# Kernel optimization log

Measured on AMD Instinct MI355X. Metric: run time of the kernel, lower is better.

The kernel has to match this reference:

```python
import jax, jax.numpy as jnp
import numpy as np

# Keras GRUCell math (reset_after=True default), weights SHARED across all
# num_layers stacked cells (faithful to `[self.rnn_cell for _ in range(L)]`).
NUM_LAYERS = 3
HID = 128


def setup_inputs() -> dict:
    key = jax.random.key(0)
    ks = jax.random.split(key, 4)
    B, T, D, H = 64, 2048, HID, HID
    s = 1.0 / np.sqrt(H)
    return {
        "X": jax.random.uniform(ks[0], (B, T, D), dtype=jnp.float32),
        "kernel": jax.random.normal(ks[1], (D, 3 * H), dtype=jnp.float32) * s,
        "rec_kernel": jax.random.normal(ks[2], (H, 3 * H), dtype=jnp.float32) * s,
        "bias_in": jnp.zeros((3 * H,), dtype=jnp.float32),
        "bias_rec": jnp.zeros((3 * H,), dtype=jnp.float32),
        "W_out": jax.random.normal(ks[3], (H, H), dtype=jnp.float32) * s,
        "b_out": jnp.zeros((H,), dtype=jnp.float32),
    }


def _gru_layer(seq_tbd, kernel, rec_kernel, bias_in, bias_rec):
    # seq_tbd: [T, B, D] -> [T, B, H]
    H = rec_kernel.shape[0]
    B = seq_tbd.shape[1]

    def step(h, x):
        gx = x @ kernel + bias_in            # [B, 3H]
        gh = h @ rec_kernel + bias_rec       # [B, 3H]
        xz, xr, xh = jnp.split(gx, 3, axis=-1)
        hz, hr, hh = jnp.split(gh, 3, axis=-1)
        z = jax.nn.sigmoid(xz + hz)          # update gate
        r = jax.nn.sigmoid(xr + hr)          # reset gate
        cand = jnp.tanh(xh + r * hh)         # candidate state
        h_new = z * h + (1.0 - z) * cand
        return h_new, h_new

    h0 = jnp.zeros((B, H), dtype=seq_tbd.dtype)
    _, out = jax.lax.scan(step, h0, seq_tbd)
    return out


def reference(X, kernel, rec_kernel, bias_in, bias_rec, W_out, b_out):
    seq = jnp.transpose(X, (1, 0, 2))  # [T, B, D]
    for _ in range(NUM_LAYERS):
        seq = _gru_layer(seq, kernel, rec_kernel, bias_in, bias_rec)
    out = jnp.transpose(seq, (1, 0, 2))  # [B, T, H]
    return jax.nn.sigmoid(out @ W_out + b_out)
```

## Files before the change

### kernel.cpp

```cpp
#include <hip/hip_runtime.h>
#include <stdint.h>

#define TSEQ 2048
#define NB   64
#define HD   128
#define G3   384
#define W_RING 128
#define SLOT_U32 (16*128)
#define RING_BYTES ((size_t)12 * W_RING * SLOT_U32 * 4)
#define FLAGS_OFF RING_BYTES

typedef __bf16 bf16_t;
typedef __bf16 bf16x8 __attribute__((ext_vector_type(8)));
typedef float  f32x4  __attribute__((ext_vector_type(4)));
typedef unsigned long long ull;

union B8 { uint4 u; bf16x8 v; unsigned a4[4]; };
union HU { bf16_t h; unsigned short u; };
static_assert(sizeof(B8) == 16, "B8 must be 16B");

__device__ __forceinline__ float fast_sigmoid(float x) {
    float e = __builtin_amdgcn_exp2f(-1.44269504f * x);
    return __builtin_amdgcn_rcpf(1.0f + e);
}
__device__ __forceinline__ float fast_tanh(float x) {
    x = fminf(9.0f, fmaxf(-9.0f, x));
    float e = __builtin_amdgcn_exp2f(2.88539008f * x);
    return 1.0f - 2.0f * __builtin_amdgcn_rcpf(1.0f + e);
}

#define MFMA16(A_, B_, C_) (C_) = __builtin_amdgcn_mfma_f32_16x16x32_bf16((A_), (B_), (C_), 0, 0, 0)

__device__ __forceinline__ void fast_barrier() {
    asm volatile("s_waitcnt lgkmcnt(0)\n\ts_barrier" ::: "memory");
}
__device__ __forceinline__ void full_barrier() {
    asm volatile("s_waitcnt vmcnt(0) lgkmcnt(0)\n\ts_barrier" ::: "memory");
}

__device__ __forceinline__ ull ld_agent_u64(const ull* p) {
    return __hip_atomic_load(p, __ATOMIC_RELAXED, __HIP_MEMORY_SCOPE_AGENT);
}
__device__ __forceinline__ void st_agent_u32(unsigned* p, unsigned v) {
    __hip_atomic_store(p, v, __ATOMIC_RELAXED, __HIP_MEMORY_SCOPE_AGENT);
}
__device__ __forceinline__ unsigned ld_flag_rlx(const unsigned* p) {
    return __hip_atomic_load(p, __ATOMIC_RELAXED, __HIP_MEMORY_SCOPE_AGENT);
}
__device__ __forceinline__ void st_flag_rel(unsigned* p, unsigned v) {
    __hip_atomic_store(p, v, __ATOMIC_RELEASE, __HIP_MEMORY_SCOPE_AGENT);
}
__device__ __forceinline__ unsigned spin_until(const unsigned* f, unsigned need,
                                               unsigned cur, bool& dead) {
    if (cur >= need) return cur;
    if (dead) return need;
    int g = 0;
    do {
        unsigned s = ld_flag_rlx(f);
        if (s >= need) { asm volatile("" ::: "memory"); return s; }
        __builtin_amdgcn_s_sleep(2);
    } while (++g < (1 << 15));
    dead = true;
    return need;
}


#define LOADRING(DST, TT2)                                                            \
    { const ull* ps = (const ull*)(rin + ((TT2) & (W_RING - 1)) * SLOT_U32) + lane64; \
      _Pragma("unroll") for (int q = 0; q < 4; ++q)                                   \
        _Pragma("unroll") for (int k = 0; k < 4; ++k)                                 \
          raw[DST][q][k] = ld_agent_u64(ps + 16 * q + k); }

#define LOADF32(DST, TT2)                                                             \
    { const float* px = px0 + (TT2) * HD;                                             \
      _Pragma("unroll") for (int q = 0; q < 4; ++q) {                                 \
        xr0[DST][q] = *(const f32x4*)(px + 32 * q + 8 * quad);                        \
        xr1[DST][q] = *(const f32x4*)(px + 32 * q + 8 * quad + 4); } }

#define GRU_STEP(TT, PV)                                                              \
  {                                                                                   \
    B8 ah[2][4];                                                                      \
    _Pragma("unroll") for (int hl = 0; hl < 2; ++hl)                                  \
      _Pragma("unroll") for (int q = 0; q < 4; ++q)                                   \
        ah[hl][q].u = ldsh[(PV) ^ 1][hl][q][lane];                                    \
    if ((((TT) & 15) == 0) && (TT) > 0 && tid == 0)                                   \
      st_flag_rel(prod_out, (unsigned)(TT) - 1u);           \
    if ((TT) > 0) {                                                                   \
      if ((int)((TT) - 1) - (int)cons_seen > W_RING - 80)                             \
        cons_seen = spin_until(cons_out, (unsigned)((TT) - 1) - (W_RING - 80),        \
                               cons_seen, dead);                                      \
      const int sb = (((TT) - 1) & (W_RING - 1)) * SLOT_U32;                          \
      _Pragma("unroll") for (int i = 0; i < 4; ++i)                                   \
        st_agent_u32(rout + sb + (4 * quad + i) * HD + cc, pend[i]);                  \
    }                                                                                 \
    B8 xhi[4], xlo[4];                                                                \
    if (IN_RING) {                                                                    \
      _Pragma("unroll") for (int q = 0; q < 4; ++q)                                   \
        _Pragma("unroll") for (int k = 0; k < 4; ++k) {                               \
          const unsigned a = (unsigned)raw[PV][q][k];                                 \
          const unsigned c = (unsigned)(raw[PV][q][k] >> 32);                         \
          xhi[q].a4[k] = (a >> 16) | (c & 0xFFFF0000u);                               \
          xlo[q].a4[k] = (a & 0xFFFFu) | (c << 16);                                   \
        }                                                                             \
    } else {                                                                          \
      _Pragma("unroll") for (int q = 0; q < 4; ++q)                                   \
        _Pragma("unroll") for (int j = 0; j < 8; ++j) {                               \
          const float f = (j < 4) ? xr0[PV][q][j] : xr1[PV][q][j - 4];                \
          const bf16_t hh = (bf16_t)f;                                                \
          xhi[q].v[j] = hh;                                                           \
          xlo[q].v[j] = (bf16_t)(f - (float)hh);                                      \
        }                                                                             \
    }                                                                                 \
    f32x4 accZ  = {bZ, bZ, bZ, bZ};                                                   \
    f32x4 accR  = {bR, bR, bR, bR};                                                   \
    f32x4 accXC = {bXC, bXC, bXC, bXC};                                               \
    f32x4 accHC = {bHC, bHC, bHC, bHC};                                               \
    _Pragma("unroll") for (int q = 0; q < 4; ++q) {     \
      MFMA16(xhi[q].v, Bi_[0][q], accZ);                                              \
      MFMA16(xhi[q].v, Bi_[1][q], accR);                                              \
      MFMA16(xhi[q].v, Bi_[2][q], accXC);                                             \
      MFMA16(xlo[q].v, Bi_[0][q], accZ);                                              \
      MFMA16(xlo[q].v, Bi_[1][q], accR);                                              \
      MFMA16(xlo[q].v, Bi_[2][q], accXC);                                             \
    }                                                                                 \
    _Pragma("unroll") for (int q = 0; q < 4; ++q) {                                   \
      MFMA16(ah[0][q].v, Br[0][q], accZ);                                             \
      MFMA16(ah[0][q].v, Br[1][q], accR);                                             \
      MFMA16(ah[0][q].v, Br[2][q], accHC);                                            \
      MFMA16(ah[1][q].v, Br[0][q], accZ);                                             \
      MFMA16(ah[1][q].v, Br[1][q], accR);                                             \
      MFMA16(ah[1][q].v, Br[2][q], accHC);                                            \
    }                                                                                 \
    _Pragma("unroll") for (int i = 0; i < 4; ++i) {                                   \
      const float zg = fast_sigmoid(accZ[i]);                                         \
      const float rg = fast_sigmoid(accR[i]);                                         \
      const float cd = fast_tanh(accXC[i] + rg * accHC[i]);                           \
      const float hn = cd + zg * (hprev[i] - cd);                                     \
      hprev[i] = hn;                                                                  \
      HU hh; hh.h = (bf16_t)hn;                                                       \
      HU hl_; hl_.h = (bf16_t)(hn - (float)hh.h);                                     \
      pend[i] = ((unsigned)hh.u << 16) | (unsigned)hl_.u;                             \
      const int mrow = 4 * quad + i;                                                  \
      ((bf16_t*)&ldsh[(PV)][0][qq][lamb + mrow])[jj] = hh.h;                          \
      ((bf16_t*)&ldsh[(PV)][1][qq][lamb + mrow])[jj] = hl_.h;                         \
    }                                                                                 \
    if ((TT) < TSEQ - 1) {      \
      if (IN_RING) {                                                                  \
        seen = spin_until(prod_in, (unsigned)(TT) + 2u, seen, dead);                  \
        LOADRING((PV) ^ 1, (TT) + 1);                                                 \
      } else {                                                                        \
        LOADF32((PV) ^ 1, (TT) + 1);                                                  \
      }                                                                               \
    }                                                                                 \
    if (IN_RING && tid == 0 && (((TT) & 7) == 7))                                     \
      st_agent_u32(cons_in, (unsigned)(TT));                                          \
    if ((((TT) + 1) & 15) == 0) full_barrier(); else fast_barrier();                  \
  }

template <bool IN_RING>
__device__ __forceinline__ void gru_stage(
    uint4 (*ldsh)[2][4][64],
    const float* __restrict__ X,
    const unsigned* __restrict__ rin,
    unsigned* __restrict__ rout,
    unsigned* prod_in, unsigned* cons_in,
    unsigned* prod_out, unsigned* cons_out,
    const float* __restrict__ Wrec, const float* __restrict__ Win,
    const float* __restrict__ bin, const float* __restrict__ brec, int b)
{
    const int tid  = threadIdx.x;
    const int w    = tid >> 6;
    const int lane = tid & 63;
    const int l15  = lane & 15;
    const int quad = lane >> 4;

    bf16x8 Br[3][4];
    bf16x8 Bi_[3][4];
#pragma unroll
    for (int g = 0; g < 3; ++g)
#pragma unroll
        for (int q = 0; q < 4; ++q) {
            const int col = 128 * g + 16 * w + l15;
#pragma unroll
            for (int j = 0; j < 8; ++j) {
                const int row = 32 * q + 8 * quad + j;
                Br[g][q][j]  = (bf16_t)Wrec[row * G3 + col];
                Bi_[g][q][j] = (bf16_t)Win[row * G3 + col];
            }
        }

    const int cc    = 16 * w + l15;
    const float bZ  = bin[cc] + brec[cc];
    const float bR  = bin[128 + cc] + brec[128 + cc];
    const float bXC = bin[256 + cc];
    const float bHC = brec[256 + cc];

    const float* px0 = IN_RING ? nullptr : (X + (size_t)(16 * b + l15) * TSEQ * HD);
    const int lane64 = l15 * 64 + 4 * quad;

    {
        uint4 z4; z4.x = z4.y = z4.z = z4.w = 0u;
        ldsh[1][tid >> 8][(tid >> 6) & 3][tid & 63] = z4;
    }
    const int qq   = cc >> 5;
    const int lamb = 16 * ((cc >> 3) & 3);
    const int jj   = cc & 7;

    float hprev[4] = {0.f, 0.f, 0.f, 0.f};
    unsigned pend[4] = {0u, 0u, 0u, 0u};
    unsigned seen = 0, cons_seen = 0;
    bool dead = false;

    ull   raw[2][4][4];
    f32x4 xr0[2][4], xr1[2][4];

    if (IN_RING) {
        seen = spin_until(prod_in, 1u, seen, dead);
        LOADRING(0, 0);
    } else {
        LOADF32(0, 0);
    }
    __syncthreads();

    for (int t = 0; t < TSEQ; t += 2) {
        GRU_STEP(t, 0)
        GRU_STEP(t + 1, 1)
    }
    {
        const int sb = ((TSEQ - 1) & (W_RING - 1)) * SLOT_U32;
#pragma unroll
        for (int i = 0; i < 4; ++i)
            st_agent_u32(rout + sb + (4 * quad + i) * HD + cc, pend[i]);
    }
    __syncthreads();
    if (tid == 0) {
        st_flag_rel(prod_out, (unsigned)TSEQ + 2u);
        if (IN_RING) st_agent_u32(cons_in, (unsigned)TSEQ);
    }
}

__device__ __forceinline__ void outproj_stage(
    const unsigned* __restrict__ rin, unsigned* prod_in, unsigned* cons_in,
    const float* __restrict__ Wout, const float* __restrict__ bout,
    float* __restrict__ out, int b)
{
    const int tid  = threadIdx.x;
    const int w    = tid >> 6;
    const int lane = tid & 63;
    const int l15  = lane & 15;
    const int quad = lane >> 4;

    bf16x8 Bw[4];
#pragma unroll
    for (int q = 0; q < 4; ++q)
#pragma unroll
        for (int j = 0; j < 8; ++j)
            Bw[q][j] = (bf16_t)Wout[(32 * q + 8 * quad + j) * HD + 16 * w + l15];
    const float bb = bout[16 * w + l15];
    const int lane64 = l15 * 64 + 4 * quad;

    ull raw[2][4][4];
    unsigned seen = 0;
    bool dead = false;
    seen = spin_until(prod_in, 1u, seen, dead);
    {
        const ull* ps = (const ull*)(rin + 0) + lane64;
#pragma unroll
        for (int q = 0; q < 4; ++q)
#pragma unroll
            for (int k = 0; k < 4; ++k) raw[0][q][k] = ld_agent_u64(ps + 16 * q + k);
    }
    for (int t = 0; t < TSEQ; ++t) {
        if (t < TSEQ - 1) {
            seen = spin_until(prod_in, (unsigned)(t + 2), seen, dead);
            const ull* ps = (const ull*)(rin + ((t + 1) & (W_RING - 1)) * SLOT_U32) + lane64;
#pragma unroll
            for (int q = 0; q < 4; ++q)
#pragma unroll
                for (int k = 0; k < 4; ++k)
                    raw[(t + 1) & 1][q][k] = ld_agent_u64(ps + 16 * q + k);
        }
        B8 ahhi[4], ahlo[4];
#pragma unroll
        for (int q = 0; q < 4; ++q)
#pragma unroll
            for (int k = 0; k < 4; ++k) {
                const ull d = raw[t & 1][q][k];
                const unsigned a = (unsigned)d;
                const unsigned c = (unsigned)(d >> 32);
                ahhi[q].a4[k] = (a >> 16) | (c & 0xFFFF0000u);
                ahlo[q].a4[k] = (a & 0xFFFFu) | (c << 16);
            }
        f32x4 acc = {bb, bb, bb, bb};
#pragma unroll
        for (int q = 0; q < 4; ++q) {
            MFMA16(ahhi[q].v, Bw[q], acc);
            MFMA16(ahlo[q].v, Bw[q], acc);
        }
#pragma unroll
        for (int i = 0; i < 4; ++i) {
            const float s = fast_sigmoid(acc[i]);
            out[(size_t)((16 * b + 4 * quad + i) * TSEQ + t) * HD + 16 * w + l15] = s;
        }
        if (tid == 0 && ((t & 7) == 7)) st_agent_u32(cons_in, (unsigned)t);
    }
}

__global__ __launch_bounds__(512, 1) void fused_gru(
    const float* __restrict__ X,
    const float* __restrict__ Wk, const float* __restrict__ Wr,
    const float* __restrict__ bi, const float* __restrict__ br,
    const float* __restrict__ Wo, const float* __restrict__ bo,
    float* __restrict__ out, unsigned char* __restrict__ ws)
{
    __shared__ uint4 ldsh[2][2][4][64];
    const int stage = blockIdx.x >> 2;
    const int b     = blockIdx.x & 3;
    unsigned* F = (unsigned*)(ws + FLAGS_OFF);
    unsigned* ring0 = (unsigned*)ws + (size_t)(0 * 4 + b) * W_RING * SLOT_U32;
    unsigned* ring1 = (unsigned*)ws + (size_t)(1 * 4 + b) * W_RING * SLOT_U32;
    unsigned* ring2 = (unsigned*)ws + (size_t)(2 * 4 + b) * W_RING * SLOT_U32;
    unsigned* p0 = F + (0 * 4 + b) * 64, *c0 = p0 + 32;
    unsigned* p1 = F + (1 * 4 + b) * 64, *c1 = p1 + 32;
    unsigned* p2 = F + (2 * 4 + b) * 64, *c2 = p2 + 32;

    if (stage == 0)
        gru_stage<false>(ldsh, X, nullptr, ring0, nullptr, nullptr, p0, c0, Wr, Wk, bi, br, b);
    else if (stage == 1)
        gru_stage<true>(ldsh, nullptr, ring0, ring1, p0, c0, p1, c1, Wr, Wk, bi, br, b);
    else if (stage == 2)
        gru_stage<true>(ldsh, nullptr, ring1, ring2, p1, c1, p2, c2, Wr, Wk, bi, br, b);
    else
        outproj_stage(ring2, p2, c2, Wo, bo, out, b);
}

extern "C" void kernel_launch(void* const* d_in, const int* in_sizes, int n_in,
                              void* d_out, int out_size, void* d_ws, size_t ws_size,
                              hipStream_t stream) {
    const float* X  = (const float*)d_in[0];
    const float* Wk = (const float*)d_in[1];
    const float* Wr = (const float*)d_in[2];
    const float* bi = (const float*)d_in[3];
    const float* br = (const float*)d_in[4];
    const float* Wo = (const float*)d_in[5];
    const float* bo = (const float*)d_in[6];
    float* out = (float*)d_out;

    if (ws_size < RING_BYTES + 4096) return;
    hipMemsetAsync((char*)d_ws + FLAGS_OFF, 0, 4096, stream);
    fused_gru<<<16, 512, 0, stream>>>(X, Wk, Wr, bi, br, Wo, bo, out,
                                      (unsigned char*)d_ws);
}
```

Before: 12.38 ms.

## Run all GRU layers and output projection in one block per batch slice

Replaces the 16-block cross-block pipeline, which passed hidden states through global-memory ring buffers with atomic flag spinning, with 4 blocks. Each block runs all three GRU layers and the output projection as a wavefront skewed by one timestep, exchanging hidden states through shared memory. X is staged into a swizzled shared buffer one step ahead, and the memset and workspace use are dropped. This removes the cross-block flag latency and global round-trips but puts roughly three times the serial MFMA and gate work into each block's per-tick critical path.

Measured after the change: 40.40 ms. 226% more time.

```diff
diff --git a/kernel.cpp b/kernel.cpp
--- a/kernel.cpp
+++ b/kernel.cpp
@@ -2,22 +2,14 @@
 #include <stdint.h>
 
 #define TSEQ 2048
-#define NB   64
 #define HD   128
 #define G3   384
-#define W_RING 128
-#define SLOT_U32 (16*128)
-#define RING_BYTES ((size_t)12 * W_RING * SLOT_U32 * 4)
-#define FLAGS_OFF RING_BYTES
 
 typedef __bf16 bf16_t;
 typedef __bf16 bf16x8 __attribute__((ext_vector_type(8)));
 typedef float  f32x4  __attribute__((ext_vector_type(4)));
-typedef unsigned long long ull;
 
 union B8 { uint4 u; bf16x8 v; unsigned a4[4]; };
-union HU { bf16_t h; unsigned short u; };
-static_assert(sizeof(B8) == 16, "B8 must be 16B");
 
 __device__ __forceinline__ float fast_sigmoid(float x) {
     float e = __builtin_amdgcn_exp2f(-1.44269504f * x);
@@ -31,151 +23,116 @@
 
 #define MFMA16(A_, B_, C_) (C_) = __builtin_amdgcn_mfma_f32_16x16x32_bf16((A_), (B_), (C_), 0, 0, 0)
 
-__device__ __forceinline__ void fast_barrier() {
-    asm volatile("s_waitcnt lgkmcnt(0)\n\ts_barrier" ::: "memory");
-}
-__device__ __forceinline__ void full_barrier() {
-    asm volatile("s_waitcnt vmcnt(0) lgkmcnt(0)\n\ts_barrier" ::: "memory");
-}
-
-__device__ __forceinline__ ull ld_agent_u64(const ull* p) {
-    return __hip_atomic_load(p, __ATOMIC_RELAXED, __HIP_MEMORY_SCOPE_AGENT);
-}
-__device__ __forceinline__ void st_agent_u32(unsigned* p, unsigned v) {
-    __hip_atomic_store(p, v, __ATOMIC_RELAXED, __HIP_MEMORY_SCOPE_AGENT);
-}
-__device__ __forceinline__ unsigned ld_flag_rlx(const unsigned* p) {
-    return __hip_atomic_load(p, __ATOMIC_RELAXED, __HIP_MEMORY_SCOPE_AGENT);
-}
-__device__ __forceinline__ void st_flag_rel(unsigned* p, unsigned v) {
-    __hip_atomic_store(p, v, __ATOMIC_RELEASE, __HIP_MEMORY_SCOPE_AGENT);
-}
-__device__ __forceinline__ unsigned spin_until(const unsigned* f, unsigned need,
-                                               unsigned cur, bool& dead) {
-    if (cur >= need) return cur;
-    if (dead) return need;
-    int g = 0;
-    do {
-        unsigned s = ld_flag_rlx(f);
-        if (s >= need) { asm volatile("" ::: "memory"); return s; }
-        __builtin_amdgcn_s_sleep(2);
-    } while (++g < (1 << 15));
-    dead = true;
-    return need;
-}
-
-
-#define LOADRING(DST, TT2)                                                            \
-    { const ull* ps = (const ull*)(rin + ((TT2) & (W_RING - 1)) * SLOT_U32) + lane64; \
-      _Pragma("unroll") for (int q = 0; q < 4; ++q)                                   \
-        _Pragma("unroll") for (int k = 0; k < 4; ++k)                                 \
-          raw[DST][q][k] = ld_agent_u64(ps + 16 * q + k); }
-
-#define LOADF32(DST, TT2)                                                             \
-    { const float* px = px0 + (TT2) * HD;                                             \
-      _Pragma("unroll") for (int q = 0; q < 4; ++q) {                                 \
-        xr0[DST][q] = *(const f32x4*)(px + 32 * q + 8 * quad);                        \
-        xr1[DST][q] = *(const f32x4*)(px + 32 * q + 8 * quad + 4); } }
-
-#define GRU_STEP(TT, PV)                                                              \
-  {                                                                                   \
-    B8 ah[2][4];                                                                      \
-    _Pragma("unroll") for (int hl = 0; hl < 2; ++hl)                                  \
-      _Pragma("unroll") for (int q = 0; q < 4; ++q)                                   \
-        ah[hl][q].u = ldsh[(PV) ^ 1][hl][q][lane];                                    \
-    if ((((TT) & 15) == 0) && (TT) > 0 && tid == 0)                                   \
-      st_flag_rel(prod_out, (unsigned)(TT) - 1u);           \
-    if ((TT) > 0) {                                                                   \
-      if ((int)((TT) - 1) - (int)cons_seen > W_RING - 80)                             \
-        cons_seen = spin_until(cons_out, (unsigned)((TT) - 1) - (W_RING - 80),        \
-                               cons_seen, dead);                                      \
-      const int sb = (((TT) - 1) & (W_RING - 1)) * SLOT_U32;                          \
-      _Pragma("unroll") for (int i = 0; i < 4; ++i)                                   \
-        st_agent_u32(rout + sb + (4 * quad + i) * HD + cc, pend[i]);                  \
-    }                                                                                 \
-    B8 xhi[4], xlo[4];                                                                \
-    if (IN_RING) {                                                                    \
-      _Pragma("unroll") for (int q = 0; q < 4; ++q)                                   \
-        _Pragma("unroll") for (int k = 0; k < 4; ++k) {                               \
-          const unsigned a = (unsigned)raw[PV][q][k];                                 \
-          const unsigned c = (unsigned)(raw[PV][q][k] >> 32);                         \
-          xhi[q].a4[k] = (a >> 16) | (c & 0xFFFF0000u);                               \
-          xlo[q].a4[k] = (a & 0xFFFFu) | (c << 16);                                   \
-        }                                                                             \
-    } else {                                                                          \
-      _Pragma("unroll") for (int q = 0; q < 4; ++q)                                   \
-        _Pragma("unroll") for (int j = 0; j < 8; ++j) {                               \
-          const float f = (j < 4) ? xr0[PV][q][j] : xr1[PV][q][j - 4];                \
-          const bf16_t hh = (bf16_t)f;                                                \
-          xhi[q].v[j] = hh;                                                           \
-          xlo[q].v[j] = (bf16_t)(f - (float)hh);                                      \
-        }                                                                             \
-    }                                                                                 \
-    f32x4 accZ  = {bZ, bZ, bZ, bZ};                                                   \
-    f32x4 accR  = {bR, bR, bR, bR};                                                   \
-    f32x4 accXC = {bXC, bXC, bXC, bXC};                                               \
-    f32x4 accHC = {bHC, bHC, bHC, bHC};                                               \
-    _Pragma("unroll") for (int q = 0; q < 4; ++q) {     \
-      MFMA16(xhi[q].v, Bi_[0][q], accZ);                                              \
-      MFMA16(xhi[q].v, Bi_[1][q], accR);                                              \
-      MFMA16(xhi[q].v, Bi_[2][q], accXC);                                             \
-      MFMA16(xlo[q].v, Bi_[0][q], accZ);                                              \
-      MFMA16(xlo[q].v, Bi_[1][q], accR);                                              \
-      MFMA16(xlo[q].v, Bi_[2][q], accXC);                                             \
-    }                                                                                 \
-    _Pragma("unroll") for (int q = 0; q < 4; ++q) {                                   \
-      MFMA16(ah[0][q].v, Br[0][q], accZ);                                             \
-      MFMA16(ah[0][q].v, Br[1][q], accR);                                             \
-      MFMA16(ah[0][q].v, Br[2][q], accHC);                                            \
-      MFMA16(ah[1][q].v, Br[0][q], accZ);                                             \
-      MFMA16(ah[1][q].v, Br[1][q], accR);                                             \
-      MFMA16(ah[1][q].v, Br[2][q], accHC);                                            \
-    }                                                                                 \
-    _Pragma("unroll") for (int i = 0; i < 4; ++i) {                                   \
-      const float zg = fast_sigmoid(accZ[i]);                                         \
-      const float rg = fast_sigmoid(accR[i]);                                         \
-      const float cd = fast_tanh(accXC[i] + rg * accHC[i]);                           \
-      const float hn = cd + zg * (hprev[i] - cd);                                     \
-      hprev[i] = hn;                                                                  \
-      HU hh; hh.h = (bf16_t)hn;                                                       \
-      HU hl_; hl_.h = (bf16_t)(hn - (float)hh.h);                                     \
-      pend[i] = ((unsigned)hh.u << 16) | (unsigned)hl_.u;                             \
-      const int mrow = 4 * quad + i;                                                  \
-      ((bf16_t*)&ldsh[(PV)][0][qq][lamb + mrow])[jj] = hh.h;                          \
-      ((bf16_t*)&ldsh[(PV)][1][qq][lamb + mrow])[jj] = hl_.h;                         \
-    }                                                                                 \
-    if ((TT) < TSEQ - 1) {      \
-      if (IN_RING) {                                                                  \
-        seen = spin_until(prod_in, (unsigned)(TT) + 2u, seen, dead);                  \
-        LOADRING((PV) ^ 1, (TT) + 1);                                                 \
-      } else {                                                                        \
-        LOADF32((PV) ^ 1, (TT) + 1);                                                  \
-      }                                                                               \
-    }                                                                                 \
-    if (IN_RING && tid == 0 && (((TT) & 7) == 7))                                     \
-      st_agent_u32(cons_in, (unsigned)(TT));                                          \
-    if ((((TT) + 1) & 15) == 0) full_barrier(); else fast_barrier();                  \
+
+#define GRU_PHASE(XH, XL, AH, AL, HP, IF, PP)                               \
+  { f32x4 accZ  = {bZ, bZ, bZ, bZ};                                         \
+    f32x4 accR  = {bR, bR, bR, bR};                                         \
+    f32x4 accXC = {bXC, bXC, bXC, bXC};                                     \
+    f32x4 accHC = {bHC, bHC, bHC, bHC};                                     \
+    _Pragma("unroll") for (int q = 0; q < 4; ++q) {                         \
+      MFMA16(XH[q].v, Bi_[0][q], accZ);                                     \
+      MFMA16(XH[q].v, Bi_[1][q], accR);                                     \
+      MFMA16(XH[q].v, Bi_[2][q], accXC);                                    \
+      MFMA16(XL[q].v, Bi_[0][q], accZ);                                     \
+      MFMA16(XL[q].v, Bi_[1][q], accR);                                     \
+      MFMA16(XL[q].v, Bi_[2][q], accXC);                                    \
+    }                                                                       \
+    _Pragma("unroll") for (int q = 0; q < 4; ++q) {                         \
+      MFMA16(AH[q].v, Br_[0][q], accZ);                                     \
+      MFMA16(AH[q].v, Br_[1][q], accR);                                     \
+      MFMA16(AH[q].v, Br_[2][q], accHC);                                    \
+      MFMA16(AL[q].v, Br_[0][q], accZ);                                     \
+      MFMA16(AL[q].v, Br_[1][q], accR);                                     \
+      MFMA16(AL[q].v, Br_[2][q], accHC);                                    \
+    }                                                                       \
+    _Pragma("unroll") for (int i = 0; i < 4; ++i) {                         \
+      const float zg = fast_sigmoid(accZ[i]);                               \
+      const float rg = fast_sigmoid(accR[i]);                               \
+      const float cd = fast_tanh(accXC[i] + rg * accHC[i]);                 \
+      const float hn = cd + zg * (HP[i] - cd);                              \
+      HP[i] = hn;                                                           \
+      const bf16_t hh = (bf16_t)hn;                                         \
+      const bf16_t hl = (bf16_t)(hn - (float)hh);                           \
+      const int mrow = 4 * quad + i;                                        \
+      ((bf16_t*)&ldsh[IF][PP][0][qq][lamb + mrow])[jj] = hh;                \
+      ((bf16_t*)&ldsh[IF][PP][1][qq][lamb + mrow])[jj] = hl;                \
+    } }
+
+#define TICK(TT, PP)                                                          \
+  {                                                                           \
+    uint4 xstage;                                                             \
+    const bool do_stage = ((TT) + 1 < TSEQ);                                  \
+    if (do_stage) xstage = *(const uint4*)(xsrc0 + (size_t)((TT) + 1) * HD);  \
+    B8 xhi[4], xlo[4];                                                        \
+    if ((TT) < TSEQ) {                                                        \
+      const char* xb = (const char*)&ldsx[PP][0];                             \
+      _Pragma("unroll") for (int q = 0; q < 4; ++q) {                         \
+        const int base = l15 * 512 + (32 * q + 8 * quad) * 4;                 \
+        const int sw   = (l15 & 7) << 4;                                      \
+        const f32x4 f0 = *(const f32x4*)(xb + (base ^ sw));                   \
+        const f32x4 f1 = *(const f32x4*)(xb + ((base + 16) ^ sw));            \
+        _Pragma("unroll") for (int j = 0; j < 4; ++j) {                       \
+          const bf16_t h0 = (bf16_t)f0[j];                                    \
+          xhi[q].v[j] = h0;                                                   \
+          xlo[q].v[j] = (bf16_t)(f0[j] - (float)h0);                          \
+          const bf16_t h1 = (bf16_t)f1[j];                                    \
+          xhi[q].v[j + 4] = h1;                                               \
+          xlo[q].v[j + 4] = (bf16_t)(f1[j] - (float)h1);                      \
+        }                                                                     \
+      }                                                                       \
+    }                                                                         \
+    B8 a0h[4], a0l[4], a1h[4], a1l[4], a2h[4], a2l[4];                        \
+    if ((TT) <= TSEQ)                                                         \
+      _Pragma("unroll") for (int q = 0; q < 4; ++q) {                         \
+        a0h[q].u = ldsh[0][(PP) ^ 1][0][q][lane];                             \
+        a0l[q].u = ldsh[0][(PP) ^ 1][1][q][lane];                             \
+      }                                                                       \
+    if ((TT) < TSEQ) GRU_PHASE(xhi, xlo, a0h, a0l, hp0, 0, PP)                \
+    if ((TT) >= 1 && (TT) <= TSEQ + 1)                                        \
+      _Pragma("unroll") for (int q = 0; q < 4; ++q) {                         \
+        a1h[q].u = ldsh[1][(PP) ^ 1][0][q][lane];                             \
+        a1l[q].u = ldsh[1][(PP) ^ 1][1][q][lane];                             \
+      }                                                                       \
+    if ((TT) >= 1 && (TT) < TSEQ + 1) GRU_PHASE(a0h, a0l, a1h, a1l, hp1, 1, PP) \
+    if ((TT) >= 2)                                                            \
+      _Pragma("unroll") for (int q = 0; q < 4; ++q) {                         \
+        a2h[q].u = ldsh[2][(PP) ^ 1][0][q][lane];                             \
+        a2l[q].u = ldsh[2][(PP) ^ 1][1][q][lane];                             \
+      }                                                                       \
+    if ((TT) >= 2 && (TT) < TSEQ + 2) GRU_PHASE(a1h, a1l, a2h, a2l, hp2, 2, PP) \
+    if ((TT) >= 3 && (TT) < TSEQ + 3) {                                       \
+      f32x4 acc = {bb, bb, bb, bb};                                           \
+      _Pragma("unroll") for (int q = 0; q < 4; ++q) {                         \
+        MFMA16(a2h[q].v, Bw[q], acc);                                         \
+        MFMA16(a2l[q].v, Bw[q], acc);                                         \
+      }                                                                       \
+      const int t3 = (TT) - 3;                                                \
+      _Pragma("unroll") for (int i = 0; i < 4; ++i)                           \
+        out[((size_t)(16 * b + 4 * quad + i) * TSEQ + t3) * HD + cc] =        \
+            fast_sigmoid(acc[i]);                                             \
+    }                                                                         \
+    if (do_stage) *(uint4*)((char*)&ldsx[(PP) ^ 1][0] + tid * 16) = xstage;   \
+    __syncthreads();                                                          \
   }
 
-template <bool IN_RING>
-__device__ __forceinline__ void gru_stage(
-    uint4 (*ldsh)[2][4][64],
+__global__ __launch_bounds__(512, 2) void fused_gru(
     const float* __restrict__ X,
-    const unsigned* __restrict__ rin,
-    unsigned* __restrict__ rout,
-    unsigned* prod_in, unsigned* cons_in,
-    unsigned* prod_out, unsigned* cons_out,
-    const float* __restrict__ Wrec, const float* __restrict__ Win,
-    const float* __restrict__ bin, const float* __restrict__ brec, int b)
+    const float* __restrict__ Wk, const float* __restrict__ Wr,
+    const float* __restrict__ bi, const float* __restrict__ br,
+    const float* __restrict__ Wo, const float* __restrict__ bo,
+    float* __restrict__ out)
 {
+    __shared__ uint4 ldsh[3][2][2][4][64];
+    __shared__ float ldsx[2][16 * HD];
+
+    const int b    = blockIdx.x;
     const int tid  = threadIdx.x;
     const int w    = tid >> 6;
     const int lane = tid & 63;
     const int l15  = lane & 15;
     const int quad = lane >> 4;
 
-    bf16x8 Br[3][4];
-    bf16x8 Bi_[3][4];
+    bf16x8 Br_[3][4], Bi_[3][4], Bw[4];
 #pragma unroll
     for (int g = 0; g < 3; ++g)
 #pragma unroll
@@ -184,154 +141,50 @@
 #pragma unroll
             for (int j = 0; j < 8; ++j) {
                 const int row = 32 * q + 8 * quad + j;
-                Br[g][q][j]  = (bf16_t)Wrec[row * G3 + col];
-                Bi_[g][q][j] = (bf16_t)Win[row * G3 + col];
+                Br_[g][q][j] = (bf16_t)Wr[row * G3 + col];
+                Bi_[g][q][j] = (bf16_t)Wk[row * G3 + col];
             }
         }
-
-    const int cc    = 16 * w + l15;
-    const float bZ  = bin[cc] + brec[cc];
-    const float bR  = bin[128 + cc] + brec[128 + cc];
-    const float bXC = bin[256 + cc];
-    const float bHC = brec[256 + cc];
-
-    const float* px0 = IN_RING ? nullptr : (X + (size_t)(16 * b + l15) * TSEQ * HD);
-    const int lane64 = l15 * 64 + 4 * quad;
-
-    {
-        uint4 z4; z4.x = z4.y = z4.z = z4.w = 0u;
-        ldsh[1][tid >> 8][(tid >> 6) & 3][tid & 63] = z4;
-    }
+#pragma unroll
+    for (int q = 0; q < 4; ++q)
+#pragma unroll
+        for (int j = 0; j < 8; ++j)
+            Bw[q][j] = (bf16_t)Wo[(32 * q + 8 * quad + j) * HD + 16 * w + l15];
+
+    const int   cc  = 16 * w + l15;
+    const float bZ  = bi[cc] + br[cc];
+    const float bR  = bi[128 + cc] + br[128 + cc];
+    const float bXC = bi[256 + cc];
+    const float bHC = br[256 + cc];
+    const float bb  = bo[cc];
+
     const int qq   = cc >> 5;
     const int lamb = 16 * ((cc >> 3) & 3);
     const int jj   = cc & 7;
 
-    float hprev[4] = {0.f, 0.f, 0.f, 0.f};
-    unsigned pend[4] = {0u, 0u, 0u, 0u};
-    unsigned seen = 0, cons_seen = 0;
-    bool dead = false;
-
-    ull   raw[2][4][4];
-    f32x4 xr0[2][4], xr1[2][4];
-
-    if (IN_RING) {
-        seen = spin_until(prod_in, 1u, seen, dead);
-        LOADRING(0, 0);
-    } else {
-        LOADF32(0, 0);
+    {
+        uint4 z4; z4.x = z4.y = z4.z = z4.w = 0u;
+        for (int i = tid; i < 3 * 2 * 2 * 4 * 64; i += 512) ((uint4*)ldsh)[i] = z4;
+    }
+
+    const int xrow = tid >> 5;
+    const int xcg  = (tid & 31) ^ (xrow & 7);
+    const float* xsrc0 = X + (size_t)(16 * b + xrow) * TSEQ * HD + 4 * xcg;
+
+    {
+        const uint4 x0 = *(const uint4*)xsrc0;
+        *(uint4*)((char*)&ldsx[0][0] + tid * 16) = x0;
     }
     __syncthreads();
 
-    for (int t = 0; t < TSEQ; t += 2) {
-        GRU_STEP(t, 0)
-        GRU_STEP(t + 1, 1)
+    float hp0[4] = {0.f, 0.f, 0.f, 0.f};
+    float hp1[4] = {0.f, 0.f, 0.f, 0.f};
+    float hp2[4] = {0.f, 0.f, 0.f, 0.f};
+
+    for (int tau = 0; tau < TSEQ + 4; tau += 2) {
+        TICK(tau, 0)
+        TICK(tau + 1, 1)
     }
-    {
-        const int sb = ((TSEQ - 1) & (W_RING - 1)) * SLOT_U32;
-#pragma unroll
-        for (int i = 0; i < 4; ++i)
-            st_agent_u32(rout + sb + (4 * quad + i) * HD + cc, pend[i]);
-    }
-    __syncthreads();
-    if (tid == 0) {
-        st_flag_rel(prod_out, (unsigned)TSEQ + 2u);
-        if (IN_RING) st_agent_u32(cons_in, (unsigned)TSEQ);
-    }
-}
-
-__device__ __forceinline__ void outproj_stage(
-    const unsigned* __restrict__ rin, unsigned* prod_in, unsigned* cons_in,
-    const float* __restrict__ Wout, const float* __restrict__ bout,
-    float* __restrict__ out, int b)
-{
-    const int tid  = threadIdx.x;
-    const int w    = tid >> 6;
-    const int lane = tid & 63;
-    const int l15  = lane & 15;
-    const int quad = lane >> 4;
-
-    bf16x8 Bw[4];
-#pragma unroll
-    for (int q = 0; q < 4; ++q)
-#pragma unroll
-        for (int j = 0; j < 8; ++j)
-            Bw[q][j] = (bf16_t)Wout[(32 * q + 8 * quad + j) * HD + 16 * w + l15];
-    const float bb = bout[16 * w + l15];
-    const int lane64 = l15 * 64 + 4 * quad;
-
-    ull raw[2][4][4];
-    unsigned seen = 0;
-    bool dead = false;
-    seen = spin_until(prod_in, 1u, seen, dead);
-    {
-        const ull* ps = (const ull*)(rin + 0) + lane64;
-#pragma unroll
-        for (int q = 0; q < 4; ++q)
-#pragma unroll
-            for (int k = 0; k < 4; ++k) raw[0][q][k] = ld_agent_u64(ps + 16 * q + k);
-    }
-    for (int t = 0; t < TSEQ; ++t) {
-        if (t < TSEQ - 1) {
-            seen = spin_until(prod_in, (unsigned)(t + 2), seen, dead);
-            const ull* ps = (const ull*)(rin + ((t + 1) & (W_RING - 1)) * SLOT_U32) + lane64;
-#pragma unroll
-            for (int q = 0; q < 4; ++q)
-#pragma unroll
-                for (int k = 0; k < 4; ++k)
-                    raw[(t + 1) & 1][q][k] = ld_agent_u64(ps + 16 * q + k);
-        }
-        B8 ahhi[4], ahlo[4];
-#pragma unroll
-        for (int q = 0; q < 4; ++q)
-#pragma unroll
-            for (int k = 0; k < 4; ++k) {
-                const ull d = raw[t & 1][q][k];
-                const unsigned a = (unsigned)d;
-                const unsigned c = (unsigned)(d >> 32);
-                ahhi[q].a4[k] = (a >> 16) | (c & 0xFFFF0000u);
-                ahlo[q].a4[k] = (a & 0xFFFFu) | (c << 16);
-            }
-        f32x4 acc = {bb, bb, bb, bb};
-#pragma unroll
-        for (int q = 0; q < 4; ++q) {
-            MFMA16(ahhi[q].v, Bw[q], acc);
-            MFMA16(ahlo[q].v, Bw[q], acc);
-        }
-#pragma unroll
-        for (int i = 0; i < 4; ++i) {
-            const float s = fast_sigmoid(acc[i]);
-            out[(size_t)((16 * b + 4 * quad + i) * TSEQ + t) * HD + 16 * w + l15] = s;
-        }
-        if (tid == 0 && ((t & 7) == 7)) st_agent_u32(cons_in, (unsigned)t);
-    }
-}
-
-__global__ __launch_bounds__(512, 1) void fused_gru(
-    const float* __restrict__ X,
-    const float* __restrict__ Wk, const float* __restrict__ Wr,
-    const float* __restrict__ bi, const float* __restrict__ br,
-    const float* __restrict__ Wo, const float* __restrict__ bo,
-    float* __restrict__ out, unsigned char* __restrict__ ws)
-{
-    __shared__ uint4 ldsh[2][2][4][64];
-    const int stage = blockIdx.x >> 2;
-    const int b     = blockIdx.x & 3;
-    unsigned* F = (unsigned*)(ws + FLAGS_OFF);
-    unsigned* ring0 = (unsigned*)ws + (size_t)(0 * 4 + b) * W_RING * SLOT_U32;
-    unsigned* ring1 = (unsigned*)ws + (size_t)(1 * 4 + b) * W_RING * SLOT_U32;
-    unsigned* ring2 = (unsigned*)ws + (size_t)(2 * 4 + b) * W_RING * SLOT_U32;
-    unsigned* p0 = F + (0 * 4 + b) * 64, *c0 = p0 + 32;
-    unsigned* p1 = F + (1 * 4 + b) * 64, *c1 = p1 + 32;
-    unsigned* p2 = F + (2 * 4 + b) * 64, *c2 = p2 + 32;
-
-    if (stage == 0)
-        gru_stage<false>(ldsh, X, nullptr, ring0, nullptr, nullptr, p0, c0, Wr, Wk, bi, br, b);
-    else if (stage == 1)
-        gru_stage<true>(ldsh, nullptr, ring0, ring1, p0, c0, p1, c1, Wr, Wk, bi, br, b);
-    else if (stage == 2)
-        gru_stage<true>(ldsh, nullptr, ring1, ring2, p1, c1, p2, c2, Wr, Wk, bi, br, b);
-    else
-        outproj_stage(ring2, p2, c2, Wo, bo, out, b);
 }
 
 extern "C" void kernel_launch(void* const* d_in, const int* in_sizes, int n_in,
@@ -345,9 +198,7 @@
     const float* Wo = (const float*)d_in[5];
     const float* bo = (const float*)d_in[6];
     float* out = (float*)d_out;
-
-    if (ws_size < RING_BYTES + 4096) return;
-    hipMemsetAsync((char*)d_ws + FLAGS_OFF, 0, 4096, stream);
-    fused_gru<<<16, 512, 0, stream>>>(X, Wk, Wr, bi, br, Wo, bo, out,
-                                      (unsigned char*)d_ws);
-}
+    (void)d_ws; (void)ws_size;
+
+    fused_gru<<<4, 512, 0, stream>>>(X, Wk, Wr, bi, br, Wo, bo, out);
+}
```
